# Kernel tuning notes

Measured on AMD Instinct MI355X. Metric: run time of the kernel, lower is better.

## Reference

```python
import jax, jax.numpy as jnp
import numpy as np

N_NODES = 100000
N_EDGES = 1000000
VOCAB = 128
EMB = 64
HID = 64
N_CLASSES = 2
N_GRAPHS = 2048


def setup_inputs() -> dict:
    key = jax.random.key(0)
    ks = jax.random.split(key, 12)
    x = jax.random.randint(ks[0], (N_NODES,), 0, VOCAB)
    edge_index = jax.random.randint(ks[1], (2, N_EDGES), 0, N_NODES)
    batch = jnp.sort(jax.random.randint(ks[2], (N_NODES,), 0, N_GRAPHS))

    def glorot(k, shape):
        fan = shape[0]
        return jax.random.normal(k, shape, dtype=jnp.float32) / np.sqrt(fan).astype(np.float32)

    emb = jax.random.normal(ks[3], (VOCAB, EMB), dtype=jnp.float32)
    W1_l = glorot(ks[4], (EMB, HID)); b1 = jnp.zeros((HID,), jnp.float32)
    W1_r = glorot(ks[5], (EMB, HID))
    W2_l = glorot(ks[6], (HID, HID)); b2 = jnp.zeros((HID,), jnp.float32)
    W2_r = glorot(ks[7], (HID, HID))
    W_out = glorot(ks[8], (HID, N_CLASSES)); b_out = jnp.zeros((N_CLASSES,), jnp.float32)
    return {"x": x, "edge_index": edge_index, "batch": batch, "emb": emb,
            "W1_l": W1_l, "b1": b1, "W1_r": W1_r,
            "W2_l": W2_l, "b2": b2, "W2_r": W2_r,
            "W_out": W_out, "b_out": b_out}


def _sage_conv(h, src, dst, Wl, bl, Wr):
    # PyG SAGEConv: out = lin_l(mean_{j in N(i)} h_j) + lin_r(h_i); lin_r has no bias
    msgs = h[src]                                                        # [E, D] gather
    agg = jax.ops.segment_sum(msgs, dst, num_segments=N_NODES)          # [N, D] scatter-add
    cnt = jax.ops.segment_sum(jnp.ones((src.shape[0], 1), h.dtype), dst,
                              num_segments=N_NODES)                      # [N, 1] degree
    mean = agg / jnp.maximum(cnt, 1.0)
    return mean @ Wl + bl + h @ Wr


def reference(x, edge_index, batch, emb, W1_l, b1, W1_r, W2_l, b2, W2_r, W_out, b_out):
    src, dst = edge_index[0], edge_index[1]
    h = emb[x]                                                           # [N, EMB]
    h = jax.nn.relu(_sage_conv(h, src, dst, W1_l, b1, W1_r))             # [N, HID]
    h = jax.nn.relu(_sage_conv(h, src, dst, W2_l, b2, W2_r))             # [N, HID]
    # global_mean_pool over graph ids
    gsum = jax.ops.segment_sum(h, batch, num_segments=N_GRAPHS)          # [G, HID]
    gcnt = jax.ops.segment_sum(jnp.ones((N_NODES, 1), h.dtype), batch,
                               num_segments=N_GRAPHS)
    pooled = gsum / jnp.maximum(gcnt, 1.0)
    return pooled @ W_out + b_out                                        # [G, C]
```

## Files before the change

### kernel.cpp

```cpp
#include <hip/hip_runtime.h>
#include <hip/hip_bf16.h>

#define N_NODES 100000
#define N_EDGES 1000000
#define EMB 64
#define HID 64
#define VOCAB 128
#define N_GRAPHS 2048

#define CBUCKET 256
#define NBK ((N_NODES + CBUCKET - 1) / CBUCKET)
#define CAP 4096
#define CHUNK 4096
#define SCAT_BLOCKS ((N_EDGES + CHUNK - 1) / CHUNK)
#define GB ((N_NODES + 255) / 256)

#define BCASTF(v, l) __int_as_float(__builtin_amdgcn_readlane(__float_as_int(v), (l)))

typedef __attribute__((ext_vector_type(8))) short short8;
typedef __attribute__((ext_vector_type(4))) float f32x4;
typedef __attribute__((ext_vector_type(2))) float f32x2;
typedef __attribute__((ext_vector_type(2))) unsigned int uint2v;

__device__ __forceinline__ float bf2f(unsigned short u) {
    return __uint_as_float((unsigned)u << 16);
}
__device__ __forceinline__ unsigned short f2bf(float f) {
    return __bfloat16_as_ushort(__float2bfloat16(f));
}

#define SWZF(x, patt) __int_as_float(__builtin_amdgcn_ds_swizzle(__float_as_int(x), (patt)))

__global__ __launch_bounds__(256) void scatter_kernel(
    const int* __restrict__ src, const int* __restrict__ dst,
    const int* __restrict__ x,
    int* __restrict__ cursor, unsigned* __restrict__ edge8,
    const int* __restrict__ batch, int* __restrict__ gstart,
    const float* __restrict__ emb, const float* __restrict__ W1l,
    const float* __restrict__ W1r,
    const float* __restrict__ W2l, const float* __restrict__ W2r,
    float* __restrict__ embW1l, float* __restrict__ embW1r,
    unsigned short* __restrict__ w2frag, unsigned char* __restrict__ p8z)
{
    __shared__ unsigned earr[CHUNK];
    __shared__ unsigned short karr[CHUNK];
    __shared__ int bcnt[NBK];
    __shared__ int bbase[NBK];
    int b = blockIdx.x;
    int t = threadIdx.x;

    if (b < SCAT_BLOCKS) {
        for (int i = t; i < NBK; i += 256) bcnt[i] = 0;
        __syncthreads();
        int e0 = b * CHUNK;
        int n = min(e0 + CHUNK, N_EDGES) - e0;
        for (int i = t; i < n; i += 256) {
            int d = dst[e0 + i];
            int s = src[e0 + i];
            int xv = x[s];
            int k = d >> 8;
            earr[i] = (unsigned)s | ((unsigned)xv << 17) | ((unsigned)(d & 255) << 24);
            karr[i] = (unsigned short)k;
            atomicAdd(&bcnt[k], 1);
        }
        __syncthreads();
        for (int i = t; i < NBK; i += 256) {
            int c = bcnt[i];
            bbase[i] = i * CAP + (c ? atomicAdd(&cursor[i], c) : 0);
            bcnt[i] = 0;
        }
        __syncthreads();
        for (int i = t; i < n; i += 256) {
            int k = karr[i];
            int off = atomicAdd(&bcnt[k], 1);
            edge8[bbase[k] + off] = earr[i];
        }
    } else if (b < SCAT_BLOCKS + GB) {
        int i = (b - SCAT_BLOCKS) * 256 + t;
        if (i >= N_NODES) return;
        int bg = batch[i];
        int bp = (i == 0) ? -1 : batch[i - 1];
        for (int g = bp + 1; g <= bg; ++g) gstart[g] = i;
        if (i == N_NODES - 1)
            for (int g = bg + 1; g <= N_GRAPHS; ++g) gstart[g] = N_NODES;
    } else {
        int vb = b - SCAT_BLOCKS - GB;
        if (vb == 0 && t < 16)
            ((unsigned*)(p8z + (size_t)N_NODES * 64))[t] = 0u;
        int wave = t >> 6, lane = t & 63;
        int v = vb * 4 + wave;
        if (v < VOCAB) {
            float er = emb[v * 64 + lane];
            float al = 0.f, ar = 0.f;
#pragma unroll 8
            for (int d = 0; d < 64; ++d) {
                float e = BCASTF(er, d);
                al += e * W1l[d * 64 + lane];
                ar += e * W1r[d * 64 + lane];
            }
            embW1l[v * 64 + lane] = al;
            embW1r[v * 64 + lane] = ar;
        }
        int g = vb * 256 + t;
        int j = g & 7, l = (g >> 3) & 63, h = (g >> 9) & 1, tt = g >> 10;
        int k = h * 32 + ((l >> 4) * 8) + j;
        int n = tt * 16 + (l & 15);
        float w = (n < 64) ? W2l[k * 64 + n] : W2r[k * 64 + (n - 64)];
        w2frag[g] = f2bf(w);
    }
}

__global__ __launch_bounds__(256) void csr_kernel(
    const unsigned* __restrict__ edge8, const int* __restrict__ cursor,
    int* __restrict__ row_start, int* __restrict__ deg, int* __restrict__ col)
{
    __shared__ int cnt[CBUCKET];
    __shared__ int scn[CBUCKET];
    int b = blockIdx.x;
    int t = threadIdx.x;
    int lo = b * CAP, hi = lo + cursor[b];
    cnt[t] = 0;
    __syncthreads();
    for (int i = lo + t; i < hi; i += 256)
        atomicAdd(&cnt[edge8[i] >> 24], 1);
    __syncthreads();
    int v = cnt[t];
    scn[t] = v;
    __syncthreads();
    for (int off = 1; off < 256; off <<= 1) {
        int tmp = (t >= off) ? scn[t - off] : 0;
        __syncthreads();
        scn[t] += tmp;
        __syncthreads();
    }
    int excl = scn[t] - v;
    int node = b * CBUCKET + t;
    if (node < N_NODES) { row_start[node] = lo + excl; deg[node] = v; }
    cnt[t] = excl;
    __syncthreads();
    for (int i = lo + t; i < hi; i += 256) {
        unsigned e = edge8[i];
        int slot = atomicAdd(&cnt[e >> 24], 1);
        col[lo + slot] = (int)(e & 0xFFFFFF);
    }
}

#define S1_NPW 8
__global__ __launch_bounds__(256) void sage1_kernel(
    const int* __restrict__ x, const float* __restrict__ embW1l,
    const float* __restrict__ embW1r, const float* __restrict__ b1,
    const int* __restrict__ row_start, const int* __restrict__ deg,
    const int* __restrict__ col, const unsigned short* __restrict__ w2frag,
    unsigned char* __restrict__ p8, unsigned short* __restrict__ q16)
{
    __shared__ float elds[VOCAB * 64];
    int t = threadIdx.x;
    for (int i = t * 4; i < VOCAB * 64; i += 1024)
        *(float4*)&elds[i] = *(const float4*)&embW1l[i];
    __syncthreads();

    int wave = t >> 6, lane = t & 63;
    int block_base = blockIdx.x * (4 * S1_NPW);
    int base_node = block_base + wave * S1_NPW;
    int c = lane & 15;
    int g = lane >> 4;
    float4 bias4 = ((const float4*)b1)[c];

    int rs[S1_NPW], dgs[S1_NPW], cidx[S1_NPW], xn[S1_NPW];
    float4 self4[S1_NPW];
#pragma unroll
    for (int n = 0; n < S1_NPW; ++n) {
        rs[n] = row_start[base_node + n];
        dgs[n] = deg[base_node + n];
        xn[n] = x[base_node + n];
    }
#pragma unroll
    for (int n = 0; n < S1_NPW; ++n) {
        cidx[n] = (lane < dgs[n]) ? col[rs[n] + lane] : 0;
        self4[n] = ((const float4*)(embW1r + xn[n] * 64))[c];
    }

    unsigned short* msbuf = (unsigned short*)elds;
    ushort4 h1row[S1_NPW];

    for (int n = 0; n < S1_NPW; ++n) {
        int dg = dgs[n];
        int dgc = (dg < 64) ? dg : 64;

        float4 a0 = {0.f,0.f,0.f,0.f}, a1 = {0.f,0.f,0.f,0.f};
        for (int j = 0; j < dgc; j += 8) {
            int jj0 = j + g, jj1 = j + 4 + g;
            int x0 = __shfl(cidx[n], jj0, 64) >> 17;
            int x1 = __shfl(cidx[n], jj1, 64) >> 17;
            float4 v0 = *(const float4*)&elds[x0 * 64 + c * 4];
            float4 v1 = *(const float4*)&elds[x1 * 64 + c * 4];
            if (jj0 < dgc) { a0.x += v0.x; a0.y += v0.y; a0.z += v0.z; a0.w += v0.w; }
            if (jj1 < dgc) { a1.x += v1.x; a1.y += v1.y; a1.z += v1.z; a1.w += v1.w; }
        }
        for (int k = 64; k < dg; ++k) {
            int cc = col[rs[n] + k] >> 17;
            float4 v = *(const float4*)&elds[cc * 64 + c * 4];
            if (g == 0) { a0.x += v.x; a0.y += v.y; a0.z += v.z; a0.w += v.w; }
        }
        float sx = a0.x + a1.x, sy = a0.y + a1.y, sz = a0.z + a1.z, sw = a0.w + a1.w;
        sx += __shfl_xor(sx, 16, 64); sx += __shfl_xor(sx, 32, 64);
        sy += __shfl_xor(sy, 16, 64); sy += __shfl_xor(sy, 32, 64);
        sz += __shfl_xor(sz, 16, 64); sz += __shfl_xor(sz, 32, 64);
        sw += __shfl_xor(sw, 16, 64); sw += __shfl_xor(sw, 32, 64);

        float inv = 1.0f / fmaxf((float)dg, 1.0f);
        h1row[n].x = f2bf(fmaxf(sx * inv + bias4.x + self4[n].x, 0.f));
        h1row[n].y = f2bf(fmaxf(sy * inv + bias4.y + self4[n].y, 0.f));
        h1row[n].z = f2bf(fmaxf(sz * inv + bias4.z + self4[n].z, 0.f));
        h1row[n].w = f2bf(fmaxf(sw * inv + bias4.w + self4[n].w, 0.f));
    }
    __syncthreads();

    if (g == 0) {
#pragma unroll
        for (int n = 0; n < S1_NPW; ++n)
            *(ushort4*)&msbuf[(wave * S1_NPW + n) * 72 + c * 4] = h1row[n];
    }
    __syncthreads();

    int grp = wave >> 1, tbase = (wave & 1) * 4;
    int m = lane & 15, quad = lane >> 4;
    int base16g = block_base + grp * 16;
    const unsigned short* arow = &msbuf[(grp * 16 + m) * 72 + quad * 8];
    short8 a0 = *(const short8*)(arow);
    short8 a1 = *(const short8*)(arow + 32);

#pragma unroll
    for (int tt = tbase; tt < tbase + 4; ++tt) {
        short8 b0 = *(const short8*)(w2frag + tt * 1024 + lane * 8);
        short8 b1v = *(const short8*)(w2frag + tt * 1024 + 512 + lane * 8);
        f32x4 acc = {0.f, 0.f, 0.f, 0.f};
        acc = __builtin_amdgcn_mfma_f32_16x16x32_bf16(a0, b0, acc, 0, 0, 0);
        acc = __builtin_amdgcn_mfma_f32_16x16x32_bf16(a1, b1v, acc, 0, 0, 0);
        int o = tt * 16 + m;
        if (o < 64) {
            int pk01 = __builtin_amdgcn_cvt_pk_fp8_f32(acc[0], acc[1], 0, false);
            int pk23 = __builtin_amdgcn_cvt_pk_fp8_f32(acc[2], acc[3], 0, false);
            p8[(base16g + quad * 4 + 0) * 64 + o] = (unsigned char)(pk01 & 0xff);
            p8[(base16g + quad * 4 + 1) * 64 + o] = (unsigned char)((pk01 >> 8) & 0xff);
            p8[(base16g + quad * 4 + 2) * 64 + o] = (unsigned char)(pk23 & 0xff);
            p8[(base16g + quad * 4 + 3) * 64 + o] = (unsigned char)((pk23 >> 8) & 0xff);
        } else {
            int oc = o & 63;
#pragma unroll
            for (int i = 0; i < 4; ++i)
                q16[(base16g + quad * 4 + i) * 64 + oc] = f2bf(acc[i]);
        }
    }
}

__global__ __launch_bounds__(256, 6) void sage2_kernel(
    const unsigned char* __restrict__ p, const unsigned short* __restrict__ q,
    const int* __restrict__ row_start, const int* __restrict__ deg,
    const int* __restrict__ col, const float* __restrict__ b2,
    const float* __restrict__ Wout, const int* __restrict__ batch,
    float* __restrict__ gsum)
{
    int t = threadIdx.x;
    int wave = t >> 6, lane = t & 63;
    int c8 = lane & 7;
    int node = (blockIdx.x * 4 + wave) * 8 + (lane >> 3);

    int rs = row_start[node];
    int dg = deg[node];
    int grp = batch[node];

    float4 accA = {0.f,0.f,0.f,0.f}, accB = {0.f,0.f,0.f,0.f};
    int r0 = 0;
    while (true) {
        int cid0 = (r0 + c8     < dg) ? (col[rs + r0 + c8    ] & 0x1FFFF) : N_NODES;
        int cid1 = (r0 + c8 + 8 < dg) ? (col[rs + r0 + c8 + 8] & 0x1FFFF) : N_NODES;

        uint2v v[16];
#define GATHER(r, cidv, slot) { \
        int i_ = __builtin_amdgcn_ds_swizzle((cidv), (((r) << 5) | 0x18)); \
        v[slot] = *(const uint2v*)(p + ((size_t)i_ << 6) + (c8 << 3)); }
        GATHER(0, cid0, 0)  GATHER(1, cid0, 1)  GATHER(2, cid0, 2)  GATHER(3, cid0, 3)
        GATHER(4, cid0, 4)  GATHER(5, cid0, 5)  GATHER(6, cid0, 6)  GATHER(7, cid0, 7)
        GATHER(0, cid1, 8)  GATHER(1, cid1, 9)  GATHER(2, cid1, 10) GATHER(3, cid1, 11)
        GATHER(4, cid1, 12) GATHER(5, cid1, 13) GATHER(6, cid1, 14) GATHER(7, cid1, 15)
#undef GATHER

#pragma unroll
        for (int r = 0; r < 16; ++r) {
            f32x2 f01 = __builtin_amdgcn_cvt_pk_f32_fp8((int)v[r].x, false);
            f32x2 f23 = __builtin_amdgcn_cvt_pk_f32_fp8((int)v[r].x, true);
            f32x2 f45 = __builtin_amdgcn_cvt_pk_f32_fp8((int)v[r].y, false);
            f32x2 f67 = __builtin_amdgcn_cvt_pk_f32_fp8((int)v[r].y, true);
            accA.x += f01.x; accA.y += f01.y; accA.z += f23.x; accA.w += f23.y;
            accB.x += f45.x; accB.y += f45.y; accB.z += f67.x; accB.w += f67.y;
        }
        r0 += 16;
        if (r0 >= dg) break;
    }

    float inv = 1.0f / fmaxf((float)dg, 1.0f);
    const float4* b2p = (const float4*)b2 + (c8 << 1);
    float4 b2a = b2p[0], b2b = b2p[1];
    short8 qv = *(const short8*)(q + ((size_t)node << 6) + (c8 << 3));
    float h0 = fmaxf(accA.x * inv + b2a.x + bf2f((unsigned short)qv[0]), 0.f);
    float h1 = fmaxf(accA.y * inv + b2a.y + bf2f((unsigned short)qv[1]), 0.f);
    float h2 = fmaxf(accA.z * inv + b2a.z + bf2f((unsigned short)qv[2]), 0.f);
    float h3 = fmaxf(accA.w * inv + b2a.w + bf2f((unsigned short)qv[3]), 0.f);
    float h4 = fmaxf(accB.x * inv + b2b.x + bf2f((unsigned short)qv[4]), 0.f);
    float h5 = fmaxf(accB.y * inv + b2b.y + bf2f((unsigned short)qv[5]), 0.f);
    float h6 = fmaxf(accB.z * inv + b2b.z + bf2f((unsigned short)qv[6]), 0.f);
    float h7 = fmaxf(accB.w * inv + b2b.w + bf2f((unsigned short)qv[7]), 0.f);

    const float4* wv = (const float4*)Wout + (c8 << 2);
    float4 wa = wv[0], wb = wv[1], wc = wv[2], wd = wv[3];
    float s0 = h0*wa.x + h1*wa.z + h2*wb.x + h3*wb.z + h4*wc.x + h5*wc.z + h6*wd.x + h7*wd.z;
    float s1 = h0*wa.y + h1*wa.w + h2*wb.y + h3*wb.w + h4*wc.y + h5*wc.w + h6*wd.y + h7*wd.w;

    s0 += SWZF(s0, 0x101F); s1 += SWZF(s1, 0x101F);
    s0 += SWZF(s0, 0x081F); s1 += SWZF(s1, 0x081F);
    s0 += SWZF(s0, 0x041F); s1 += SWZF(s1, 0x041F);
    if (c8 == 0) {
        atomicAdd(&gsum[(grp << 1) + 0], s0);
        atomicAdd(&gsum[(grp << 1) + 1], s1);
    }
}

__global__ __launch_bounds__(256) void finalize_kernel(
    const float* __restrict__ gsum, const int* __restrict__ gstart,
    const float* __restrict__ bout, float* __restrict__ out)
{
    int g = blockIdx.x * 256 + threadIdx.x;
    if (g >= N_GRAPHS) return;
    int cnt = gstart[g + 1] - gstart[g];
    float inv = 1.0f / fmaxf((float)cnt, 1.0f);
    out[g * 2 + 0] = gsum[g * 2 + 0] * inv + bout[0];
    out[g * 2 + 1] = gsum[g * 2 + 1] * inv + bout[1];
}

extern "C" void kernel_launch(void* const* d_in, const int* in_sizes, int n_in,
                              void* d_out, int out_size, void* d_ws, size_t ws_size,
                              hipStream_t stream) {
    const int*   x    = (const int*)  d_in[0];
    const int*   ei   = (const int*)  d_in[1];
    const int*   batch= (const int*)  d_in[2];
    const float* emb  = (const float*)d_in[3];
    const float* W1l  = (const float*)d_in[4];
    const float* b1   = (const float*)d_in[5];
    const float* W1r  = (const float*)d_in[6];
    const float* W2l  = (const float*)d_in[7];
    const float* b2   = (const float*)d_in[8];
    const float* W2r  = (const float*)d_in[9];
    const float* Wout = (const float*)d_in[10];
    const float* bout = (const float*)d_in[11];
    float* out = (float*)d_out;

    const int* src = ei;
    const int* dst = ei + N_EDGES;

    char* ws = (char*)d_ws;
    size_t off = 0;
    unsigned char*  p8     = (unsigned char*) (ws + off); off += (size_t)N_NODES * 64 + 64;
    unsigned short* q16    = (unsigned short*)(ws + off); off += (size_t)N_NODES * 64 * 2;
    unsigned short* w2frag = (unsigned short*)(ws + off); off += (size_t)8192 * 2;
    float*    embW1l = (float*)   (ws + off); off += (size_t)VOCAB * 64 * 4;
    float*    embW1r = (float*)   (ws + off); off += (size_t)VOCAB * 64 * 4;
    int*      rowst  = (int*)     (ws + off); off += (size_t)N_NODES * 4;
    int*      deg    = (int*)     (ws + off); off += (size_t)N_NODES * 4;
    int*      col    = (int*)     (ws + off); off += (size_t)(NBK * CAP + 256) * 4;
    unsigned* edge8  = (unsigned*)(ws + off); off += (size_t)NBK * CAP * 4;
    int*      gstart = (int*)     (ws + off); off += (size_t)(N_GRAPHS + 1) * 4;
    int*      cursor = (int*)     (ws + off); off += (size_t)NBK * 4;
    float*    gsum   = (float*)   (ws + off); off += (size_t)N_GRAPHS * 2 * 4;

    hipMemsetAsync(cursor, 0, (size_t)NBK * 4 + (size_t)N_GRAPHS * 2 * 4, stream);

    scatter_kernel<<<SCAT_BLOCKS + GB + 32, 256, 0, stream>>>(
        src, dst, x, cursor, edge8,
        batch, gstart, emb, W1l, W1r, W2l, W2r, embW1l, embW1r, w2frag, p8);
    csr_kernel<<<NBK, 256, 0, stream>>>(edge8, cursor, rowst, deg, col);
    sage1_kernel<<<N_NODES / (4 * S1_NPW), 256, 0, stream>>>(
        x, embW1l, embW1r, b1, rowst, deg, col, w2frag, p8, q16);
    sage2_kernel<<<N_NODES / 32, 256, 0, stream>>>(
        p8, q16, rowst, deg, col, b2, Wout, batch, gsum);
    finalize_kernel<<<(N_GRAPHS + 255) / 256, 256, 0, stream>>>(gsum, gstart, bout, out);
}
```

Baseline: 222.1 us.

## Aggregate layer-2 messages via bucketed edge list with shared-memory atomics

The second SAGE layer no longer walks per-node CSR rows. It now reads the destination-bucketed edge8 list directly: each block owns half of a 256-node bucket, scans every edge in that bucket, gathers full 64-byte fp8 source rows, and accumulates them into a swizzled shared-memory buffer with LDS float atomics. A per-node epilogue then applies the mean, bias, residual, ReLU and output projection. This trades the CSR indirection and irregular per-node loop lengths for 64 LDS atomics per edge, and each block reads every edge in its bucket twice while discarding the other half's. Summation order also changes.

```diff
diff --git a/kernel.cpp b/kernel.cpp
--- a/kernel.cpp
+++ b/kernel.cpp
@@ -20,7 +20,6 @@
 typedef __attribute__((ext_vector_type(8))) short short8;
 typedef __attribute__((ext_vector_type(4))) float f32x4;
 typedef __attribute__((ext_vector_type(2))) float f32x2;
-typedef __attribute__((ext_vector_type(2))) unsigned int uint2v;
 
 __device__ __forceinline__ float bf2f(unsigned short u) {
     return __uint_as_float((unsigned)u << 16);
@@ -28,8 +27,6 @@
 __device__ __forceinline__ unsigned short f2bf(float f) {
     return __bfloat16_as_ushort(__float2bfloat16(f));
 }
-
-#define SWZF(x, patt) __int_as_float(__builtin_amdgcn_ds_swizzle(__float_as_int(x), (patt)))
 
 __global__ __launch_bounds__(256) void scatter_kernel(
     const int* __restrict__ src, const int* __restrict__ dst,
@@ -254,75 +251,77 @@
     }
 }
 
-__global__ __launch_bounds__(256, 6) void sage2_kernel(
+#define S2B_NODES 128
+__global__ __launch_bounds__(256) void sage2_kernel(
     const unsigned char* __restrict__ p, const unsigned short* __restrict__ q,
-    const int* __restrict__ row_start, const int* __restrict__ deg,
-    const int* __restrict__ col, const float* __restrict__ b2,
+    const unsigned* __restrict__ edge8, const int* __restrict__ cursor,
+    const int* __restrict__ deg, const float* __restrict__ b2,
     const float* __restrict__ Wout, const int* __restrict__ batch,
     float* __restrict__ gsum)
 {
+    __shared__ float acc[S2B_NODES * 64];
+    int blk = blockIdx.x;
+    int bucket = blk >> 1;
+    int half = blk & 1;
     int t = threadIdx.x;
-    int wave = t >> 6, lane = t & 63;
-    int c8 = lane & 7;
-    int node = (blockIdx.x * 4 + wave) * 8 + (lane >> 3);
-
-    int rs = row_start[node];
-    int dg = deg[node];
-    int grp = batch[node];
-
-    float4 accA = {0.f,0.f,0.f,0.f}, accB = {0.f,0.f,0.f,0.f};
-    int r0 = 0;
-    while (true) {
-        int cid0 = (r0 + c8     < dg) ? (col[rs + r0 + c8    ] & 0x1FFFF) : N_NODES;
-        int cid1 = (r0 + c8 + 8 < dg) ? (col[rs + r0 + c8 + 8] & 0x1FFFF) : N_NODES;
-
-        uint2v v[16];
-#define GATHER(r, cidv, slot) { \
-        int i_ = __builtin_amdgcn_ds_swizzle((cidv), (((r) << 5) | 0x18)); \
-        v[slot] = *(const uint2v*)(p + ((size_t)i_ << 6) + (c8 << 3)); }
-        GATHER(0, cid0, 0)  GATHER(1, cid0, 1)  GATHER(2, cid0, 2)  GATHER(3, cid0, 3)
-        GATHER(4, cid0, 4)  GATHER(5, cid0, 5)  GATHER(6, cid0, 6)  GATHER(7, cid0, 7)
-        GATHER(0, cid1, 8)  GATHER(1, cid1, 9)  GATHER(2, cid1, 10) GATHER(3, cid1, 11)
-        GATHER(4, cid1, 12) GATHER(5, cid1, 13) GATHER(6, cid1, 14) GATHER(7, cid1, 15)
-#undef GATHER
-
-#pragma unroll
-        for (int r = 0; r < 16; ++r) {
-            f32x2 f01 = __builtin_amdgcn_cvt_pk_f32_fp8((int)v[r].x, false);
-            f32x2 f23 = __builtin_amdgcn_cvt_pk_f32_fp8((int)v[r].x, true);
-            f32x2 f45 = __builtin_amdgcn_cvt_pk_f32_fp8((int)v[r].y, false);
-            f32x2 f67 = __builtin_amdgcn_cvt_pk_f32_fp8((int)v[r].y, true);
-            accA.x += f01.x; accA.y += f01.y; accA.z += f23.x; accA.w += f23.y;
-            accB.x += f45.x; accB.y += f45.y; accB.z += f67.x; accB.w += f67.y;
-        }
-        r0 += 16;
-        if (r0 >= dg) break;
-    }
-
-    float inv = 1.0f / fmaxf((float)dg, 1.0f);
-    const float4* b2p = (const float4*)b2 + (c8 << 1);
-    float4 b2a = b2p[0], b2b = b2p[1];
-    short8 qv = *(const short8*)(q + ((size_t)node << 6) + (c8 << 3));
-    float h0 = fmaxf(accA.x * inv + b2a.x + bf2f((unsigned short)qv[0]), 0.f);
-    float h1 = fmaxf(accA.y * inv + b2a.y + bf2f((unsigned short)qv[1]), 0.f);
-    float h2 = fmaxf(accA.z * inv + b2a.z + bf2f((unsigned short)qv[2]), 0.f);
-    float h3 = fmaxf(accA.w * inv + b2a.w + bf2f((unsigned short)qv[3]), 0.f);
-    float h4 = fmaxf(accB.x * inv + b2b.x + bf2f((unsigned short)qv[4]), 0.f);
-    float h5 = fmaxf(accB.y * inv + b2b.y + bf2f((unsigned short)qv[5]), 0.f);
-    float h6 = fmaxf(accB.z * inv + b2b.z + bf2f((unsigned short)qv[6]), 0.f);
-    float h7 = fmaxf(accB.w * inv + b2b.w + bf2f((unsigned short)qv[7]), 0.f);
-
-    const float4* wv = (const float4*)Wout + (c8 << 2);
-    float4 wa = wv[0], wb = wv[1], wc = wv[2], wd = wv[3];
-    float s0 = h0*wa.x + h1*wa.z + h2*wb.x + h3*wb.z + h4*wc.x + h5*wc.z + h6*wd.x + h7*wd.z;
-    float s1 = h0*wa.y + h1*wa.w + h2*wb.y + h3*wb.w + h4*wc.y + h5*wc.w + h6*wd.y + h7*wd.w;
-
-    s0 += SWZF(s0, 0x101F); s1 += SWZF(s1, 0x101F);
-    s0 += SWZF(s0, 0x081F); s1 += SWZF(s1, 0x081F);
-    s0 += SWZF(s0, 0x041F); s1 += SWZF(s1, 0x041F);
-    if (c8 == 0) {
-        atomicAdd(&gsum[(grp << 1) + 0], s0);
-        atomicAdd(&gsum[(grp << 1) + 1], s1);
+
+    for (int i = t * 4; i < S2B_NODES * 64; i += 1024)
+        *(float4*)&acc[i] = (float4){0.f, 0.f, 0.f, 0.f};
+    __syncthreads();
+
+    int lo = bucket * CAP;
+    int ecnt = cursor[bucket];
+
+    for (int i = t; i < ecnt; i += 256) {
+        unsigned e = edge8[lo + i];
+        int ld = (int)(e >> 24);
+        if ((ld >> 7) != half) continue;
+        int srcn = (int)(e & 0x1FFFF);
+        int r = ld & (S2B_NODES - 1);
+        const uint4* row = (const uint4*)(p + ((size_t)srcn << 6));
+        uint4 w0 = row[0], w1 = row[1], w2 = row[2], w3 = row[3];
+        float* ap = &acc[r * 64];
+        int s4 = (r & 15) << 2;
+#define ADD4(word, kb) { \
+        f32x2 lo_ = __builtin_amdgcn_cvt_pk_f32_fp8((int)(word), false); \
+        f32x2 hi_ = __builtin_amdgcn_cvt_pk_f32_fp8((int)(word), true);  \
+        float* gp_ = ap + ((kb) ^ s4); \
+        atomicAdd(gp_ + 0, lo_.x); atomicAdd(gp_ + 1, lo_.y); \
+        atomicAdd(gp_ + 2, hi_.x); atomicAdd(gp_ + 3, hi_.y); }
+        ADD4(w0.x,  0) ADD4(w0.y,  4) ADD4(w0.z,  8) ADD4(w0.w, 12)
+        ADD4(w1.x, 16) ADD4(w1.y, 20) ADD4(w1.z, 24) ADD4(w1.w, 28)
+        ADD4(w2.x, 32) ADD4(w2.y, 36) ADD4(w2.z, 40) ADD4(w2.w, 44)
+        ADD4(w3.x, 48) ADD4(w3.y, 52) ADD4(w3.z, 56) ADD4(w3.w, 60)
+#undef ADD4
+    }
+    __syncthreads();
+
+    if (t < S2B_NODES) {
+        int node = bucket * CBUCKET + half * S2B_NODES + t;
+        if (node < N_NODES) {
+            int dg = deg[node];
+            int grp = batch[node];
+            float inv = 1.0f / fmaxf((float)dg, 1.0f);
+            const float* ap = &acc[t * 64];
+            int s4 = (t & 15) << 2;
+            float s0 = 0.f, s1 = 0.f;
+#pragma unroll
+            for (int j = 0; j < 16; ++j) {
+                float4 v = *(const float4*)(ap + ((j << 2) ^ s4));
+                float4 bb = ((const float4*)b2)[j];
+                ushort4 qv = *(const ushort4*)(q + ((size_t)node << 6) + (j << 2));
+                float4 wA = ((const float4*)Wout)[j * 2];
+                float4 wB = ((const float4*)Wout)[j * 2 + 1];
+                float h0 = fmaxf(v.x * inv + bb.x + bf2f(qv.x), 0.f);
+                float h1 = fmaxf(v.y * inv + bb.y + bf2f(qv.y), 0.f);
+                float h2 = fmaxf(v.z * inv + bb.z + bf2f(qv.z), 0.f);
+                float h3 = fmaxf(v.w * inv + bb.w + bf2f(qv.w), 0.f);
+                s0 += h0 * wA.x + h1 * wA.z + h2 * wB.x + h3 * wB.z;
+                s1 += h0 * wA.y + h1 * wA.w + h2 * wB.y + h3 * wB.w;
+            }
+            atomicAdd(&gsum[(grp << 1) + 0], s0);
+            atomicAdd(&gsum[(grp << 1) + 1], s1);
+        }
     }
 }
 
@@ -381,7 +380,7 @@
     csr_kernel<<<NBK, 256, 0, stream>>>(edge8, cursor, rowst, deg, col);
     sage1_kernel<<<N_NODES / (4 * S1_NPW), 256, 0, stream>>>(
         x, embW1l, embW1r, b1, rowst, deg, col, w2frag, p8, q16);
-    sage2_kernel<<<N_NODES / 32, 256, 0, stream>>>(
-        p8, q16, rowst, deg, col, b2, Wout, batch, gsum);
+    sage2_kernel<<<NBK * 2, 256, 0, stream>>>(
+        p8, q16, edge8, cursor, deg, b2, Wout, batch, gsum);
     finalize_kernel<<<(N_GRAPHS + 255) / 256, 256, 0, stream>>>(gsum, gstart, bout, out);
 }
```

New measurement: 589.5 us. +165.4%, slower.
